# Kernel tuning notes

Hardware: AMD Instinct MI355X
Metric: run time of the kernel (lower is better)

## Reference

```python
import jax, jax.numpy as jnp
import numpy as np

ALIGN_CORNERS = True
APPLY_SMOOTHSTEP = True

SIZES = [(32, 32, 32), (64, 64, 64), (128, 128, 128), (256, 256, 256)]
FEAT_DIMS = [4, 4, 4, 4]
N_POINTS = 1048576  # 2**20 sample points (e.g. 8192 rays x 128 samples)


def setup_inputs() -> dict:
    key = jax.random.key(0)
    ks = jax.random.split(key, 1 + len(SIZES))
    # grid_sample-style coords in [-1, 1], layout [1, 1, 1, N, 3] (x, y, z)
    grid = jax.random.uniform(ks[0], (1, 1, 1, N_POINTS, 3), dtype=jnp.float32) * 2.0 - 1.0
    inp = {"grid": grid}
    for i, (size, c) in enumerate(zip(SIZES, FEAT_DIMS)):
        # original init: (rand(1,C,1,1,1)*2-1).repeat over spatial; use randn volumes for a
        # non-degenerate baseline (same shapes/math path)
        inp[f"vol{i}"] = jax.random.normal(ks[1 + i], (1, c, *size), dtype=jnp.float32)
    return inp


def _smooth_sample(vol, grid_pts):
    """Trilinear sample with border padding, align_corners=True, smoothstep weights.

    vol: [C, D, H, W]; grid_pts: [P, 3] with (x, y, z) in [-1, 1].
    Returns [C, P].
    """
    C, D, H, W = vol.shape
    # unnormalize (align_corners=True): [-1,1] -> [0, dim-1]; border padding via clip
    x = jnp.clip((grid_pts[:, 0] + 1.0) * 0.5 * (W - 1), 0.0, W - 1)
    y = jnp.clip((grid_pts[:, 1] + 1.0) * 0.5 * (H - 1), 0.0, H - 1)
    z = jnp.clip((grid_pts[:, 2] + 1.0) * 0.5 * (D - 1), 0.0, D - 1)

    x0 = jnp.floor(x); y0 = jnp.floor(y); z0 = jnp.floor(z)
    tx = x - x0; ty = y - y0; tz = z - z0
    if APPLY_SMOOTHSTEP:
        tx = tx * tx * (3.0 - 2.0 * tx)
        ty = ty * ty * (3.0 - 2.0 * ty)
        tz = tz * tz * (3.0 - 2.0 * tz)

    x0i = x0.astype(jnp.int32); x1i = jnp.minimum(x0i + 1, W - 1)
    y0i = y0.astype(jnp.int32); y1i = jnp.minimum(y0i + 1, H - 1)
    z0i = z0.astype(jnp.int32); z1i = jnp.minimum(z0i + 1, D - 1)

    # 8 corner gathers -> [C, P]
    c000 = vol[:, z0i, y0i, x0i]; c001 = vol[:, z0i, y0i, x1i]
    c010 = vol[:, z0i, y1i, x0i]; c011 = vol[:, z0i, y1i, x1i]
    c100 = vol[:, z1i, y0i, x0i]; c101 = vol[:, z1i, y0i, x1i]
    c110 = vol[:, z1i, y1i, x0i]; c111 = vol[:, z1i, y1i, x1i]

    c00 = c000 + (c001 - c000) * tx
    c01 = c010 + (c011 - c010) * tx
    c10 = c100 + (c101 - c100) * tx
    c11 = c110 + (c111 - c110) * tx
    c0 = c00 + (c01 - c00) * ty
    c1 = c10 + (c11 - c10) * ty
    return c0 + (c1 - c0) * tz


def reference(grid, vol0, vol1, vol2, vol3):
    # grid: [1, 1, 1, N, 3] -> [N, 3]
    pts = grid.reshape(-1, 3)
    n = pts.shape[0]
    out = []
    for vol in (vol0, vol1, vol2, vol3):
        feat = _smooth_sample(vol[0], pts)            # [C, N]
        out.append(feat.reshape(1, -1, 1, 1, n))      # grid_sample output layout
    return jnp.concatenate(out, axis=1)               # [1, sum(C), 1, 1, N]
```

## Files before the change

### kernel.cpp

```cpp
#include <hip/hip_runtime.h>

#define NPTS 1048576

__device__ __forceinline__ float4 lerp4(const float4 a, const float4 b, const float t) {
    return make_float4(a.x + (b.x - a.x) * t,
                       a.y + (b.y - a.y) * t,
                       a.z + (b.z - a.z) * t,
                       a.w + (b.w - a.w) * t);
}

template<int D>
__device__ __forceinline__ void coords(float g, float& t, int& i0, int& i1) {
    float x = (g + 1.0f) * (0.5f * (float)(D - 1));
    x = fminf(fmaxf(x, 0.0f), (float)(D - 1));
    float x0f = floorf(x);
    t = x - x0f;
    t = t * t * (3.0f - 2.0f * t);
    i0 = (int)x0f;
    i1 = min(i0 + 1, D - 1);
}

template<int D>
__device__ __forceinline__ float4 sample_inter(const float4* __restrict__ v,
                                               float gx, float gy, float gz) {
    float tx, ty, tz; int x0, x1, y0, y1, z0, z1;
    coords<D>(gx, tx, x0, x1);
    coords<D>(gy, ty, y0, y1);
    coords<D>(gz, tz, z0, z1);
    const int b00 = (z0 * D + y0) * D;
    const int b01 = (z0 * D + y1) * D;
    const int b10 = (z1 * D + y0) * D;
    const int b11 = (z1 * D + y1) * D;
    float4 c000 = v[b00 + x0], c001 = v[b00 + x1];
    float4 c010 = v[b01 + x0], c011 = v[b01 + x1];
    float4 c100 = v[b10 + x0], c101 = v[b10 + x1];
    float4 c110 = v[b11 + x0], c111 = v[b11 + x1];
    float4 c00 = lerp4(c000, c001, tx);
    float4 c01 = lerp4(c010, c011, tx);
    float4 c10 = lerp4(c100, c101, tx);
    float4 c11 = lerp4(c110, c111, tx);
    float4 c0 = lerp4(c00, c01, ty);
    float4 c1 = lerp4(c10, c11, ty);
    return lerp4(c0, c1, tz);
}

template<int D>
__device__ __forceinline__ float4 sample_direct(const float* __restrict__ v,
                                                float gx, float gy, float gz) {
    float tx, ty, tz; int x0, x1, y0, y1, z0, z1;
    coords<D>(gx, tx, x0, x1);
    coords<D>(gy, ty, y0, y1);
    coords<D>(gz, tz, z0, z1);
    const int b00 = (z0 * D + y0) * D;
    const int b01 = (z0 * D + y1) * D;
    const int b10 = (z1 * D + y0) * D;
    const int b11 = (z1 * D + y1) * D;
    float r[4];
#pragma unroll
    for (int c = 0; c < 4; ++c) {
        const float* __restrict__ vc = v + (size_t)c * (D * D * D);
        float c000 = vc[b00 + x0], c001 = vc[b00 + x1];
        float c010 = vc[b01 + x0], c011 = vc[b01 + x1];
        float c100 = vc[b10 + x0], c101 = vc[b10 + x1];
        float c110 = vc[b11 + x0], c111 = vc[b11 + x1];
        float c00 = c000 + (c001 - c000) * tx;
        float c01 = c010 + (c011 - c010) * tx;
        float c10 = c100 + (c101 - c100) * tx;
        float c11 = c110 + (c111 - c110) * tx;
        float c0 = c00 + (c01 - c00) * ty;
        float c1 = c10 + (c11 - c10) * ty;
        r[c] = c0 + (c1 - c0) * tz;
    }
    return make_float4(r[0], r[1], r[2], r[3]);
}

template<int DHW>
__global__ __launch_bounds__(256) void xpose_kernel(const float* __restrict__ in,
                                                    float4* __restrict__ out) {
    int v = blockIdx.x * blockDim.x + threadIdx.x;
    if (v < DHW)
        out[v] = make_float4(in[v], in[v + DHW], in[v + 2 * DHW], in[v + 3 * DHW]);
}

__global__ __launch_bounds__(256) void mg_inter_kernel(
    const float* __restrict__ grid,
    const float4* __restrict__ w0, const float4* __restrict__ w1,
    const float4* __restrict__ w2, const float* __restrict__ v3,
    float* __restrict__ out)
{
    int p = blockIdx.x * blockDim.x + threadIdx.x;
    float gx = grid[3 * p + 0];
    float gy = grid[3 * p + 1];
    float gz = grid[3 * p + 2];
    float4 f0 = sample_inter<32>(w0, gx, gy, gz);
    float4 f1 = sample_inter<64>(w1, gx, gy, gz);
    float4 f2 = sample_inter<128>(w2, gx, gy, gz);
    float4 f3 = sample_direct<256>(v3, gx, gy, gz);
    out[ 0 * NPTS + p] = f0.x; out[ 1 * NPTS + p] = f0.y;
    out[ 2 * NPTS + p] = f0.z; out[ 3 * NPTS + p] = f0.w;
    out[ 4 * NPTS + p] = f1.x; out[ 5 * NPTS + p] = f1.y;
    out[ 6 * NPTS + p] = f1.z; out[ 7 * NPTS + p] = f1.w;
    out[ 8 * NPTS + p] = f2.x; out[ 9 * NPTS + p] = f2.y;
    out[10 * NPTS + p] = f2.z; out[11 * NPTS + p] = f2.w;
    out[12 * NPTS + p] = f3.x; out[13 * NPTS + p] = f3.y;
    out[14 * NPTS + p] = f3.z; out[15 * NPTS + p] = f3.w;
}

__global__ __launch_bounds__(256) void mg_direct_kernel(
    const float* __restrict__ grid,
    const float* __restrict__ v0, const float* __restrict__ v1,
    const float* __restrict__ v2, const float* __restrict__ v3,
    float* __restrict__ out)
{
    int p = blockIdx.x * blockDim.x + threadIdx.x;
    float gx = grid[3 * p + 0];
    float gy = grid[3 * p + 1];
    float gz = grid[3 * p + 2];
    float4 f0 = sample_direct<32>(v0, gx, gy, gz);
    float4 f1 = sample_direct<64>(v1, gx, gy, gz);
    float4 f2 = sample_direct<128>(v2, gx, gy, gz);
    float4 f3 = sample_direct<256>(v3, gx, gy, gz);
    out[ 0 * NPTS + p] = f0.x; out[ 1 * NPTS + p] = f0.y;
    out[ 2 * NPTS + p] = f0.z; out[ 3 * NPTS + p] = f0.w;
    out[ 4 * NPTS + p] = f1.x; out[ 5 * NPTS + p] = f1.y;
    out[ 6 * NPTS + p] = f1.z; out[ 7 * NPTS + p] = f1.w;
    out[ 8 * NPTS + p] = f2.x; out[ 9 * NPTS + p] = f2.y;
    out[10 * NPTS + p] = f2.z; out[11 * NPTS + p] = f2.w;
    out[12 * NPTS + p] = f3.x; out[13 * NPTS + p] = f3.y;
    out[14 * NPTS + p] = f3.z; out[15 * NPTS + p] = f3.w;
}

extern "C" void kernel_launch(void* const* d_in, const int* in_sizes, int n_in,
                              void* d_out, int out_size, void* d_ws, size_t ws_size,
                              hipStream_t stream) {
    const float* grid = (const float*)d_in[0];
    const float* v0   = (const float*)d_in[1];
    const float* v1   = (const float*)d_in[2];
    const float* v2   = (const float*)d_in[3];
    const float* v3   = (const float*)d_in[4];
    float* out = (float*)d_out;

    constexpr int DHW0 = 32 * 32 * 32;
    constexpr int DHW1 = 64 * 64 * 64;
    constexpr int DHW2 = 128 * 128 * 128;
    constexpr size_t WS_NEED = (size_t)(DHW0 + DHW1 + DHW2) * 16;

    const int threads = 256;
    const int pt_blocks = NPTS / threads;

    if (ws_size >= WS_NEED) {
        float4* w0 = (float4*)d_ws;
        float4* w1 = w0 + DHW0;
        float4* w2 = w1 + DHW1;
        xpose_kernel<DHW0><<<DHW0 / threads, threads, 0, stream>>>(v0, w0);
        xpose_kernel<DHW1><<<DHW1 / threads, threads, 0, stream>>>(v1, w1);
        xpose_kernel<DHW2><<<DHW2 / threads, threads, 0, stream>>>(v2, w2);
        mg_inter_kernel<<<pt_blocks, threads, 0, stream>>>(grid, w0, w1, w2, v3, out);
    } else {
        mg_direct_kernel<<<pt_blocks, threads, 0, stream>>>(grid, v0, v1, v2, v3, out);
    }
}
```

Before: 807.8 us.

## Sort sample points into spatial bins before trilinear gathers for cache locality

Adds a counting sort of the points into a 32^3 spatial bin grid (histogram, single-block scan, atomic scatter). The gather kernel then samples all four volumes in sorted order, so neighbouring threads hit nearby voxels and the random cache misses on the large volumes should drop. Each sorted block's results go to a workspace buffer, and a final permute kernel writes them back in the original point order. The cost is several extra passes over the points, global atomics, a serial single-block scan, and about 100 MB more workspace. The fast path only runs when the workspace is large enough, otherwise the old path is used.

```diff
diff --git a/kernel.cpp b/kernel.cpp
--- a/kernel.cpp
+++ b/kernel.cpp
@@ -1,6 +1,9 @@
 #include <hip/hip_runtime.h>
 
 #define NPTS 1048576
+#define NB 32
+#define NBINS (NB * NB * NB)
+
 
 __device__ __forceinline__ float4 lerp4(const float4 a, const float4 b, const float t) {
     return make_float4(a.x + (b.x - a.x) * t,
@@ -74,6 +77,7 @@
     return make_float4(r[0], r[1], r[2], r[3]);
 }
 
+
 template<int DHW>
 __global__ __launch_bounds__(256) void xpose_kernel(const float* __restrict__ in,
                                                     float4* __restrict__ out) {
@@ -81,6 +85,106 @@
     if (v < DHW)
         out[v] = make_float4(in[v], in[v + DHW], in[v + 2 * DHW], in[v + 3 * DHW]);
 }
+
+
+__device__ __forceinline__ int bin_of(float gx, float gy, float gz) {
+    float ux = fminf(fmaxf((gx + 1.0f) * 0.5f, 0.0f), 1.0f);
+    float uy = fminf(fmaxf((gy + 1.0f) * 0.5f, 0.0f), 1.0f);
+    float uz = fminf(fmaxf((gz + 1.0f) * 0.5f, 0.0f), 1.0f);
+    int bx = min((int)(ux * (float)NB), NB - 1);
+    int by = min((int)(uy * (float)NB), NB - 1);
+    int bz = min((int)(uz * (float)NB), NB - 1);
+    return (bz * NB + by) * NB + bx;
+}
+
+__global__ __launch_bounds__(256) void bin_hist_kernel(const float* __restrict__ grid,
+                                                       int* __restrict__ bins,
+                                                       unsigned* __restrict__ hist) {
+    int p = blockIdx.x * blockDim.x + threadIdx.x;
+    float gx = grid[3 * p + 0];
+    float gy = grid[3 * p + 1];
+    float gz = grid[3 * p + 2];
+    int b = bin_of(gx, gy, gz);
+    bins[p] = b;
+    atomicAdd(&hist[b], 1u);
+}
+
+__global__ __launch_bounds__(1024) void scan_kernel(const unsigned* __restrict__ hist,
+                                                    unsigned* __restrict__ offsets) {
+    __shared__ unsigned partial[1024];
+    const int t = threadIdx.x;
+    const int base = t * 32;
+    unsigned sum = 0;
+#pragma unroll
+    for (int i = 0; i < 32; ++i) sum += hist[base + i];
+    partial[t] = sum;
+    __syncthreads();
+    for (int off = 1; off < 1024; off <<= 1) {
+        unsigned v = (t >= off) ? partial[t - off] : 0u;
+        __syncthreads();
+        partial[t] += v;
+        __syncthreads();
+    }
+    unsigned run = partial[t] - sum;
+#pragma unroll
+    for (int i = 0; i < 32; ++i) {
+        offsets[base + i] = run;
+        run += hist[base + i];
+    }
+}
+
+__global__ __launch_bounds__(256) void scatter_kernel(const float* __restrict__ grid,
+                                                      const int* __restrict__ bins,
+                                                      unsigned* __restrict__ offsets,
+                                                      float4* __restrict__ sorted,
+                                                      int* __restrict__ inv) {
+    int p = blockIdx.x * blockDim.x + threadIdx.x;
+    int b = bins[p];
+    unsigned pos = atomicAdd(&offsets[b], 1u);
+    float gx = grid[3 * p + 0];
+    float gy = grid[3 * p + 1];
+    float gz = grid[3 * p + 2];
+    sorted[pos] = make_float4(gx, gy, gz, __int_as_float(p));
+    inv[p] = (int)pos;
+}
+
+
+__global__ __launch_bounds__(256) void gather_sorted_kernel(
+    const float4* __restrict__ sorted,
+    const float4* __restrict__ w0, const float4* __restrict__ w1,
+    const float4* __restrict__ w2, const float* __restrict__ v3,
+    float4* __restrict__ wsout)
+{
+    int bid = blockIdx.x;
+    int sb = (bid & 7) * (int)(gridDim.x >> 3) + (bid >> 3);
+    int s = sb * 256 + (int)threadIdx.x;
+    float4 gp = sorted[s];
+    float gx = gp.x, gy = gp.y, gz = gp.z;
+    float4 f0 = sample_inter<32>(w0, gx, gy, gz);
+    float4 f1 = sample_inter<64>(w1, gx, gy, gz);
+    float4 f2 = sample_inter<128>(w2, gx, gy, gz);
+    float4 f3 = sample_direct<256>(v3, gx, gy, gz);
+    float4* w = wsout + (size_t)s * 4;
+    w[0] = f0; w[1] = f1; w[2] = f2; w[3] = f3;
+}
+
+__global__ __launch_bounds__(256) void permute_kernel(const float4* __restrict__ wsout,
+                                                      const int* __restrict__ inv,
+                                                      float* __restrict__ out) {
+    int p = blockIdx.x * blockDim.x + threadIdx.x;
+    int s = inv[p];
+    const float4* w = wsout + (size_t)s * 4;
+    float4 f0 = w[0], f1 = w[1], f2 = w[2], f3 = w[3];
+    out[ 0 * NPTS + p] = f0.x; out[ 1 * NPTS + p] = f0.y;
+    out[ 2 * NPTS + p] = f0.z; out[ 3 * NPTS + p] = f0.w;
+    out[ 4 * NPTS + p] = f1.x; out[ 5 * NPTS + p] = f1.y;
+    out[ 6 * NPTS + p] = f1.z; out[ 7 * NPTS + p] = f1.w;
+    out[ 8 * NPTS + p] = f2.x; out[ 9 * NPTS + p] = f2.y;
+    out[10 * NPTS + p] = f2.z; out[11 * NPTS + p] = f2.w;
+    out[12 * NPTS + p] = f3.x; out[13 * NPTS + p] = f3.y;
+    out[14 * NPTS + p] = f3.z; out[15 * NPTS + p] = f3.w;
+}
+
 
 __global__ __launch_bounds__(256) void mg_inter_kernel(
     const float* __restrict__ grid,
@@ -130,6 +234,7 @@
     out[14 * NPTS + p] = f3.z; out[15 * NPTS + p] = f3.w;
 }
 
+
 extern "C" void kernel_launch(void* const* d_in, const int* in_sizes, int n_in,
                               void* d_out, int out_size, void* d_ws, size_t ws_size,
                               hipStream_t stream) {
@@ -143,12 +248,44 @@
     constexpr int DHW0 = 32 * 32 * 32;
     constexpr int DHW1 = 64 * 64 * 64;
     constexpr int DHW2 = 128 * 128 * 128;
-    constexpr size_t WS_NEED = (size_t)(DHW0 + DHW1 + DHW2) * 16;
+
+    constexpr size_t OFF_WSOUT  = 0;
+    constexpr size_t OFF_SORTED = OFF_WSOUT  + (size_t)NPTS * 64;
+    constexpr size_t OFF_W2     = OFF_SORTED + (size_t)NPTS * 16;
+    constexpr size_t OFF_W1     = OFF_W2     + (size_t)DHW2 * 16;
+    constexpr size_t OFF_W0     = OFF_W1     + (size_t)DHW1 * 16;
+    constexpr size_t OFF_BINS   = OFF_W0     + (size_t)DHW0 * 16;
+    constexpr size_t OFF_INV    = OFF_BINS   + (size_t)NPTS * 4;
+    constexpr size_t OFF_HIST   = OFF_INV    + (size_t)NPTS * 4;
+    constexpr size_t OFF_OFFS   = OFF_HIST   + (size_t)NBINS * 4;
+    constexpr size_t WS_FULL    = OFF_OFFS   + (size_t)NBINS * 4;
+    constexpr size_t WS_INTER   = (size_t)(DHW0 + DHW1 + DHW2) * 16;
 
     const int threads = 256;
     const int pt_blocks = NPTS / threads;
-
-    if (ws_size >= WS_NEED) {
+    char* ws = (char*)d_ws;
+
+    if (ws_size >= WS_FULL) {
+        float4*   wsout  = (float4*)(ws + OFF_WSOUT);
+        float4*   sorted = (float4*)(ws + OFF_SORTED);
+        float4*   w2     = (float4*)(ws + OFF_W2);
+        float4*   w1     = (float4*)(ws + OFF_W1);
+        float4*   w0     = (float4*)(ws + OFF_W0);
+        int*      bins   = (int*)   (ws + OFF_BINS);
+        int*      inv    = (int*)   (ws + OFF_INV);
+        unsigned* hist   = (unsigned*)(ws + OFF_HIST);
+        unsigned* offs   = (unsigned*)(ws + OFF_OFFS);
+
+        hipMemsetAsync(hist, 0, (size_t)NBINS * 4, stream);
+        xpose_kernel<DHW0><<<DHW0 / threads, threads, 0, stream>>>(v0, w0);
+        xpose_kernel<DHW1><<<DHW1 / threads, threads, 0, stream>>>(v1, w1);
+        xpose_kernel<DHW2><<<DHW2 / threads, threads, 0, stream>>>(v2, w2);
+        bin_hist_kernel<<<pt_blocks, threads, 0, stream>>>(grid, bins, hist);
+        scan_kernel<<<1, 1024, 0, stream>>>(hist, offs);
+        scatter_kernel<<<pt_blocks, threads, 0, stream>>>(grid, bins, offs, sorted, inv);
+        gather_sorted_kernel<<<pt_blocks, threads, 0, stream>>>(sorted, w0, w1, w2, v3, wsout);
+        permute_kernel<<<pt_blocks, threads, 0, stream>>>(wsout, inv, out);
+    } else if (ws_size >= WS_INTER) {
         float4* w0 = (float4*)d_ws;
         float4* w1 = w0 + DHW0;
         float4* w2 = w1 + DHW1;
```

New measurement: 705.6 us. -12.6%, faster.
